# Kernel tuning notes

Measured on AMD Instinct MI355X. Metric: run time of the kernel, lower is better.

Reference implementation:

```python
import jax, jax.numpy as jnp
import numpy as np

B, C, N_OUT = 8, 64, 65536
N_IN = 262144  # unpooled (input) spatial size
K, P = 9, 4    # kernel_size, bilinear interp points


def setup_inputs() -> dict:
    key = jax.random.key(0)
    k1, k2, k3, k4 = jax.random.split(key, 4)
    x = jax.random.normal(k1, (B, C, N_OUT), dtype=jnp.float32)
    idx_mask = jax.random.randint(k2, (B, C, N_OUT), 0, K, dtype=jnp.int32)
    sample_map = jax.random.randint(k3, (N_OUT, K, P), 0, N_IN, dtype=jnp.int32)
    interp_weights = jax.random.uniform(k4, (N_OUT, K, P), dtype=jnp.float32)
    return {"x": x, "idx_mask": idx_mask, "sample_map": sample_map,
            "interp_weights": interp_weights}


def reference(x, idx_mask, sample_map, interp_weights):
    # x: [B,C,N_out] pooled values; idx_mask: [B,C,N_out] winning kernel tap
    # sample_map: [N_out,K,P] int indices into flattened unpooled domain
    # interp_weights: [N_out,K,P] interpolation weights
    b, c, n_out = x.shape
    o_idx = jnp.arange(n_out)[None, None, :]               # [1,1,N_out]
    sel_map = sample_map[o_idx, idx_mask]                  # [B,C,N_out,P]
    sel_w = interp_weights[o_idx, idx_mask]                # [B,C,N_out,P]
    contrib = sel_w * x[..., None]                         # [B,C,N_out,P]
    out = jnp.zeros((b, c, N_IN), dtype=x.dtype)
    bi = jnp.arange(b)[:, None, None, None]
    ci = jnp.arange(c)[None, :, None, None]
    out = out.at[bi, ci, sel_map].add(contrib)             # scatter-add unpool
    return out
```

## Files before the change

kernel.cpp:

```cpp
#include <hip/hip_runtime.h>

#define BB      8
#define CC      64
#define N_OUT   65536
#define N_IN    262144
#define KK      9
#define PP      4
#define NE      (N_OUT * KK * PP)
#define NPLANES 512
#define CHUNK   32
#define NCHUNKS (N_IN / CHUNK)
#define GTH     512
#define NW      (GTH / 64)
#define NFB     128
#define EPB     (NE / NFB)

#define WS_OFFSETS 0
#define WS_TOT     8208
#define WS_PRIV    16400
#define WS_HDR     (16400 + NFB * 8192)
#define WS_ENTR    (1064976 + N_OUT * KK)
#define WS_XK      (1654800 + 4 * NE)
#define WS_END     (11091984 + N_OUT * 512)

#define XKTILE 16
#define XPAD   520
__global__ __launch_bounds__(256) void k_xk(const float* __restrict__ x,
                                            const int*   __restrict__ idx,
                                            unsigned* __restrict__ xk,
                                            unsigned* __restrict__ hdr) {
    __shared__ float xs[XKTILE * XPAD];
    __shared__ unsigned char ks[XKTILE * XPAD];
    __shared__ unsigned ot[XKTILE * 512];
    __shared__ int cnt[XKTILE][12];
    __shared__ int cur[XKTILE][12];
    const int t = threadIdx.x;
    const int obase = blockIdx.x * XKTILE;

    for (int i = t; i < XKTILE * 12; i += 256) cnt[i / 12][i % 12] = 0;

    for (int i = t; i < 512 * (XKTILE / 4); i += 256) {
        int p = i >> 2, q = i & 3;
        const size_t g = (size_t)p * N_OUT + obase + 4 * q;
        float4 xv = *(const float4*)(x + g);
        int4   kv = *(const int4*)(idx + g);
        int b = (4 * q) * XPAD + p;
        xs[b] = xv.x; xs[b + XPAD] = xv.y; xs[b + 2 * XPAD] = xv.z; xs[b + 3 * XPAD] = xv.w;
        ks[b] = (unsigned char)kv.x; ks[b + XPAD] = (unsigned char)kv.y;
        ks[b + 2 * XPAD] = (unsigned char)kv.z; ks[b + 3 * XPAD] = (unsigned char)kv.w;
    }
    __syncthreads();
    for (int i = t; i < XKTILE * 512; i += 256) {
        int oo = i >> 9, p = i & 511;
        atomicAdd(&cnt[oo][ks[oo * XPAD + p]], 1);
    }
    __syncthreads();
    if (t < XKTILE) {
        int s = 0;
        for (int k = 0; k < KK; ++k) {
            int c = cnt[t][k];
            cur[t][k] = s;
            hdr[(size_t)(obase + t) * KK + k] = (unsigned)(s | (c << 16));
            s += c;
        }
    }
    __syncthreads();
    for (int i = t; i < XKTILE * 512; i += 256) {
        int oo = i >> 9, p = i & 511;
        int k = ks[oo * XPAD + p];
        int pos = atomicAdd(&cur[oo][k], 1);
        unsigned xb = __float_as_uint(xs[oo * XPAD + p]);
        ot[(oo << 9) + pos] = (xb & 0xFFFFFE00u) | (unsigned)p;
    }
    __syncthreads();
    for (int i = t; i < XKTILE * 128; i += 256) {
        int oo = i >> 7, c4 = i & 127;
        ((int4*)(xk + (((size_t)(obase + oo)) << 9)))[c4] = ((const int4*)(ot + (oo << 9)))[c4];
    }
}

__global__ __launch_bounds__(1024) void k_histA(const int* __restrict__ smap,
                                                int* __restrict__ priv) {
    __shared__ int h[8192];
    const int b = blockIdx.x;
    const int t = threadIdx.x;
    for (int i = t; i < 8192; i += 1024) h[i] = 0;
    __syncthreads();
    const int e0 = b * EPB;
    #pragma unroll 4
    for (int i = 0; i < EPB / 1024; ++i)
        atomicAdd(&h[smap[e0 + i * 1024 + t] >> 5], 1);
    __syncthreads();
    for (int i = t; i < 8192; i += 1024) priv[b * 8192 + i] = h[i];
}

__global__ __launch_bounds__(1024) void k_colscan(int* __restrict__ priv,
                                                  int* __restrict__ tot) {
    const int key = blockIdx.x * 1024 + threadIdx.x;
    int run = 0;
    for (int b = 0; b < NFB; ++b) {
        int* p = priv + b * 8192 + key;
        int v = *p; *p = run; run += v;
    }
    tot[key] = run;
}

__global__ __launch_bounds__(1024) void k_scan8k(const int* __restrict__ counts,
                                                 int* __restrict__ offsets) {
    __shared__ int sw[1024];
    const int t = threadIdx.x;
    int4 a = ((const int4*)counts)[2 * t];
    int4 b = ((const int4*)counts)[2 * t + 1];
    int s = a.x + a.y + a.z + a.w + b.x + b.y + b.z + b.w;
    sw[t] = s;
    __syncthreads();
    for (int off = 1; off < 1024; off <<= 1) {
        int v = (t >= off) ? sw[t - off] : 0;
        __syncthreads();
        sw[t] += v;
        __syncthreads();
    }
    int run = sw[t] - s;
    int vals[8] = {a.x, a.y, a.z, a.w, b.x, b.y, b.z, b.w};
    int o[8];
    #pragma unroll
    for (int q = 0; q < 8; ++q) { o[q] = run; run += vals[q]; }
    ((int4*)offsets)[2 * t]     = make_int4(o[0], o[1], o[2], o[3]);
    ((int4*)offsets)[2 * t + 1] = make_int4(o[4], o[5], o[6], o[7]);
    if (t == 1023) offsets[8192] = NE;
}

__global__ __launch_bounds__(1024) void k_fillB(const int* __restrict__ smap,
                                                const float* __restrict__ wts,
                                                const int* __restrict__ priv,
                                                const int* __restrict__ offsets,
                                                const unsigned* __restrict__ hdr,
                                                int4* __restrict__ entries) {
    __shared__ int cur[8192];
    const int b = blockIdx.x;
    const int t = threadIdx.x;
    for (int i = t; i < 8192; i += 1024) cur[i] = offsets[i] + priv[b * 8192 + i];
    __syncthreads();
    const int e0 = b * EPB;
    for (int i = 0; i < EPB / 1024; ++i) {
        const int e = e0 + i * 1024 + t;
        const int n = smap[e];
        const int o = e / 36;
        const int r = e - o * 36;
        const int k = r >> 2;
        const unsigned h = hdr[(size_t)o * KK + k];
        const int pos = atomicAdd(&cur[n >> 5], 1);
        entries[pos] = make_int4((o << 5) | (n & 31), __float_as_int(wts[e]), (int)h, 0);
    }
}

__global__ __launch_bounds__(GTH) void k_gather5(const int* __restrict__ offsets,
                                                 const int4* __restrict__ entries,
                                                 const unsigned* __restrict__ xk,
                                                 float* __restrict__ out) {
    __shared__ float acc[CHUNK * NPLANES];
    const int bid = blockIdx.x;
    const int c = (bid & 7) * (NCHUNKS / 8) + (bid >> 3);
    const int tid = threadIdx.x;
    const int lane = tid & 63;
    const int wid = tid >> 6;

    float4* a4 = (float4*)acc;
    for (int i = tid; i < CHUNK * NPLANES / 4; i += GTH) a4[i] = float4{0.f, 0.f, 0.f, 0.f};
    __syncthreads();

    const int j1 = offsets[c + 1];
    int j = offsets[c] + wid;
    int4 e = make_int4(0, 0, 0, 0);
    unsigned u0 = 0;
    bool have = (j < j1);
    if (have) {
        e = entries[j];
        int o = ((unsigned)e.x) >> 5;
        int st = e.z & 0xFFFF;
        int cn = ((unsigned)e.z) >> 16;
        if (lane < cn) u0 = xk[((size_t)o << 9) + st + lane];
    }
    while (have) {
        const int jn = j + NW;
        const bool hn = (jn < j1);
        int4 en = make_int4(0, 0, 0, 0);
        unsigned un = 0;
        if (hn) {
            en = entries[jn];
            int on = ((unsigned)en.x) >> 5;
            int stn = en.z & 0xFFFF;
            int cnn = ((unsigned)en.z) >> 16;
            if (lane < cnn) un = xk[((size_t)on << 9) + stn + lane];
        }
        {
            const int nl = e.x & 31;
            const float w = __int_as_float(e.y);
            const int cn = ((unsigned)e.z) >> 16;
            if (lane < cn) {
                int p = u0 & 511;
                float xv = __int_as_float(u0 & 0xFFFFFE00u);
                atomicAdd(&acc[(nl << 9) + (p ^ nl)], w * xv);
            }
            if (cn > 64) {
                const int o = ((unsigned)e.x) >> 5;
                const int st = e.z & 0xFFFF;
                for (int b = lane + 64; b < cn; b += 64) {
                    unsigned u = xk[((size_t)o << 9) + st + b];
                    int p = u & 511;
                    float xv = __int_as_float(u & 0xFFFFFE00u);
                    atomicAdd(&acc[(nl << 9) + (p ^ nl)], w * xv);
                }
            }
        }
        e = en; u0 = un; j = jn; have = hn;
    }
    __syncthreads();

    const int n0 = c << 5;
    for (int i = tid; i < CHUNK * NPLANES / 4; i += GTH) {
        const int p = i >> 3;
        const int nl = (i & 7) << 2;
        float4 v;
        v.x = acc[((nl + 0) << 9) + (p ^ (nl + 0))];
        v.y = acc[((nl + 1) << 9) + (p ^ (nl + 1))];
        v.z = acc[((nl + 2) << 9) + (p ^ (nl + 2))];
        v.w = acc[((nl + 3) << 9) + (p ^ (nl + 3))];
        *(float4*)(out + (size_t)p * N_IN + n0 + nl) = v;
    }
}

__global__ __launch_bounds__(256) void zero_kernel(float4* __restrict__ out, int n4) {
    int i = blockIdx.x * blockDim.x + threadIdx.x;
    int stride = gridDim.x * blockDim.x;
    const float4 z = {0.f, 0.f, 0.f, 0.f};
    for (; i < n4; i += stride) out[i] = z;
}

__global__ __launch_bounds__(256) void scatter_kernel(
    const float* __restrict__ x, const int* __restrict__ idx_mask,
    const int4* __restrict__ smap, const float4* __restrict__ wts,
    float* __restrict__ out)
{
    const int plane = blockIdx.x >> 8;
    const int o = ((blockIdx.x & 255) << 8) + threadIdx.x;
    const long ibase = (long)plane * N_OUT + o;
    const float xv = x[ibase];
    const int k = idx_mask[ibase];
    const int row = o * KK + k;
    const int4 m = smap[row];
    const float4 w = wts[row];
    float* op = out + (long)plane * N_IN;
    atomicAdd(op + m.x, w.x * xv);
    atomicAdd(op + m.y, w.y * xv);
    atomicAdd(op + m.z, w.z * xv);
    atomicAdd(op + m.w, w.w * xv);
}

extern "C" void kernel_launch(void* const* d_in, const int* in_sizes, int n_in,
                              void* d_out, int out_size, void* d_ws, size_t ws_size,
                              hipStream_t stream) {
    const float* x    = (const float*)d_in[0];
    const int*   idx  = (const int*)d_in[1];
    const int*   smap = (const int*)d_in[2];
    const float* wts  = (const float*)d_in[3];
    float* out = (float*)d_out;

    if (ws_size < (size_t)WS_END * 4) {
        zero_kernel<<<4096, 256, 0, stream>>>((float4*)out, out_size / 4);
        scatter_kernel<<<NPLANES * (N_OUT / 256), 256, 0, stream>>>(
            x, idx, (const int4*)smap, (const float4*)wts, out);
        return;
    }

    int* ws = (int*)d_ws;
    int* offsets   = ws + WS_OFFSETS;
    int* tot       = ws + WS_TOT;
    int* priv      = ws + WS_PRIV;
    unsigned* hdr  = (unsigned*)(ws + WS_HDR);
    int4* entries  = (int4*)(ws + WS_ENTR);
    unsigned* xk   = (unsigned*)(ws + WS_XK);

    k_xk<<<N_OUT / XKTILE, 256, 0, stream>>>(x, idx, xk, hdr);
    k_histA<<<NFB, 1024, 0, stream>>>(smap, priv);
    k_colscan<<<8, 1024, 0, stream>>>(priv, tot);
    k_scan8k<<<1, 1024, 0, stream>>>(tot, offsets);
    k_fillB<<<NFB, 1024, 0, stream>>>(smap, wts, priv, offsets, hdr, entries);
    k_gather5<<<NCHUNKS, GTH, 0, stream>>>(offsets, entries, xk, out);
}
```

Baseline: 1.012 ms.

## Halve gather chunk size, deepen entry prefetch, and retune LDS swizzle

Chunk width drops from 32 to 16 output columns, so the gather kernel's LDS accumulator halves (32KB) and more blocks can reside per CU, with launch bounds asking for 8. The histogram, scan and fill kernels are resized for twice as many keys. The gather loop now handles two entries per warp per iteration with a deeper software pipeline (entries two steps ahead, xk values one step ahead, including the second 64-lane slice), and the LDS swizzle is changed. The cost is more blocks, more per-chunk overhead, a larger scan, and higher register pressure.

```diff
diff --git a/kernel.cpp b/kernel.cpp
--- a/kernel.cpp
+++ b/kernel.cpp
@@ -8,20 +8,21 @@
 #define PP      4
 #define NE      (N_OUT * KK * PP)
 #define NPLANES 512
-#define CHUNK   32
+#define CHUNK   16
 #define NCHUNKS (N_IN / CHUNK)
+#define NKEY    NCHUNKS
 #define GTH     512
 #define NW      (GTH / 64)
 #define NFB     128
 #define EPB     (NE / NFB)
 
 #define WS_OFFSETS 0
-#define WS_TOT     8208
-#define WS_PRIV    16400
-#define WS_HDR     (16400 + NFB * 8192)
-#define WS_ENTR    (1064976 + N_OUT * KK)
-#define WS_XK      (1654800 + 4 * NE)
-#define WS_END     (11091984 + N_OUT * 512)
+#define WS_TOT     16400
+#define WS_PRIV    32784
+#define WS_HDR     (32784 + NFB * NKEY)
+#define WS_ENTR    (2129936 + N_OUT * KK)
+#define WS_XK      (2719760 + 4 * NE)
+#define WS_END     (12156944 + N_OUT * 512)
 
 #define XKTILE 16
 #define XPAD   520
@@ -81,17 +82,17 @@
 
 __global__ __launch_bounds__(1024) void k_histA(const int* __restrict__ smap,
                                                 int* __restrict__ priv) {
-    __shared__ int h[8192];
+    __shared__ int h[NKEY];
     const int b = blockIdx.x;
     const int t = threadIdx.x;
-    for (int i = t; i < 8192; i += 1024) h[i] = 0;
+    for (int i = t; i < NKEY; i += 1024) h[i] = 0;
     __syncthreads();
     const int e0 = b * EPB;
-    #pragma unroll 4
+    #pragma unroll 2
     for (int i = 0; i < EPB / 1024; ++i)
-        atomicAdd(&h[smap[e0 + i * 1024 + t] >> 5], 1);
-    __syncthreads();
-    for (int i = t; i < 8192; i += 1024) priv[b * 8192 + i] = h[i];
+        atomicAdd(&h[smap[e0 + i * 1024 + t] >> 4], 1);
+    __syncthreads();
+    for (int i = t; i < NKEY; i += 1024) priv[b * NKEY + i] = h[i];
 }
 
 __global__ __launch_bounds__(1024) void k_colscan(int* __restrict__ priv,
@@ -99,19 +100,25 @@
     const int key = blockIdx.x * 1024 + threadIdx.x;
     int run = 0;
     for (int b = 0; b < NFB; ++b) {
-        int* p = priv + b * 8192 + key;
+        int* p = priv + b * NKEY + key;
         int v = *p; *p = run; run += v;
     }
     tot[key] = run;
 }
 
-__global__ __launch_bounds__(1024) void k_scan8k(const int* __restrict__ counts,
-                                                 int* __restrict__ offsets) {
+__global__ __launch_bounds__(1024) void k_scan16k(const int* __restrict__ tot,
+                                                  int* __restrict__ offsets) {
     __shared__ int sw[1024];
     const int t = threadIdx.x;
-    int4 a = ((const int4*)counts)[2 * t];
-    int4 b = ((const int4*)counts)[2 * t + 1];
-    int s = a.x + a.y + a.z + a.w + b.x + b.y + b.z + b.w;
+    int4 q0 = ((const int4*)tot)[4 * t + 0];
+    int4 q1 = ((const int4*)tot)[4 * t + 1];
+    int4 q2 = ((const int4*)tot)[4 * t + 2];
+    int4 q3 = ((const int4*)tot)[4 * t + 3];
+    int vals[16] = {q0.x, q0.y, q0.z, q0.w, q1.x, q1.y, q1.z, q1.w,
+                    q2.x, q2.y, q2.z, q2.w, q3.x, q3.y, q3.z, q3.w};
+    int s = 0;
+    #pragma unroll
+    for (int i = 0; i < 16; ++i) s += vals[i];
     sw[t] = s;
     __syncthreads();
     for (int off = 1; off < 1024; off <<= 1) {
@@ -121,13 +128,14 @@
         __syncthreads();
     }
     int run = sw[t] - s;
-    int vals[8] = {a.x, a.y, a.z, a.w, b.x, b.y, b.z, b.w};
-    int o[8];
+    int o[16];
     #pragma unroll
-    for (int q = 0; q < 8; ++q) { o[q] = run; run += vals[q]; }
-    ((int4*)offsets)[2 * t]     = make_int4(o[0], o[1], o[2], o[3]);
-    ((int4*)offsets)[2 * t + 1] = make_int4(o[4], o[5], o[6], o[7]);
-    if (t == 1023) offsets[8192] = NE;
+    for (int i = 0; i < 16; ++i) { o[i] = run; run += vals[i]; }
+    ((int4*)offsets)[4 * t + 0] = make_int4(o[0], o[1], o[2], o[3]);
+    ((int4*)offsets)[4 * t + 1] = make_int4(o[4], o[5], o[6], o[7]);
+    ((int4*)offsets)[4 * t + 2] = make_int4(o[8], o[9], o[10], o[11]);
+    ((int4*)offsets)[4 * t + 3] = make_int4(o[12], o[13], o[14], o[15]);
+    if (t == 1023) offsets[NKEY] = NE;
 }
 
 __global__ __launch_bounds__(1024) void k_fillB(const int* __restrict__ smap,
@@ -136,10 +144,10 @@
                                                 const int* __restrict__ offsets,
                                                 const unsigned* __restrict__ hdr,
                                                 int4* __restrict__ entries) {
-    __shared__ int cur[8192];
+    __shared__ int cur[NKEY];
     const int b = blockIdx.x;
     const int t = threadIdx.x;
-    for (int i = t; i < 8192; i += 1024) cur[i] = offsets[i] + priv[b * 8192 + i];
+    for (int i = t; i < NKEY; i += 1024) cur[i] = offsets[i] + priv[b * NKEY + i];
     __syncthreads();
     const int e0 = b * EPB;
     for (int i = 0; i < EPB / 1024; ++i) {
@@ -149,15 +157,16 @@
         const int r = e - o * 36;
         const int k = r >> 2;
         const unsigned h = hdr[(size_t)o * KK + k];
-        const int pos = atomicAdd(&cur[n >> 5], 1);
-        entries[pos] = make_int4((o << 5) | (n & 31), __float_as_int(wts[e]), (int)h, 0);
-    }
-}
-
-__global__ __launch_bounds__(GTH) void k_gather5(const int* __restrict__ offsets,
-                                                 const int4* __restrict__ entries,
-                                                 const unsigned* __restrict__ xk,
-                                                 float* __restrict__ out) {
+        const int pos = atomicAdd(&cur[n >> 4], 1);
+        entries[pos] = make_int4((o << 4) | (n & 15), __float_as_int(wts[e]), (int)h, 0);
+    }
+}
+
+#define SWZ(p, nl) ((p) ^ ((nl) << 1))
+__global__ __launch_bounds__(GTH, 8) void k_gather6(const int* __restrict__ offsets,
+                                                    const int4* __restrict__ entries,
+                                                    const unsigned* __restrict__ xk,
+                                                    float* __restrict__ out) {
     __shared__ float acc[CHUNK * NPLANES];
     const int bid = blockIdx.x;
     const int c = (bid & 7) * (NCHUNKS / 8) + (bid >> 3);
@@ -170,62 +179,104 @@
     __syncthreads();
 
     const int j1 = offsets[c + 1];
-    int j = offsets[c] + wid;
-    int4 e = make_int4(0, 0, 0, 0);
-    unsigned u0 = 0;
-    bool have = (j < j1);
-    if (have) {
-        e = entries[j];
-        int o = ((unsigned)e.x) >> 5;
-        int st = e.z & 0xFFFF;
-        int cn = ((unsigned)e.z) >> 16;
-        if (lane < cn) u0 = xk[((size_t)o << 9) + st + lane];
-    }
-    while (have) {
-        const int jn = j + NW;
-        const bool hn = (jn < j1);
-        int4 en = make_int4(0, 0, 0, 0);
-        unsigned un = 0;
-        if (hn) {
-            en = entries[jn];
-            int on = ((unsigned)en.x) >> 5;
-            int stn = en.z & 0xFFFF;
-            int cnn = ((unsigned)en.z) >> 16;
-            if (lane < cnn) un = xk[((size_t)on << 9) + stn + lane];
-        }
-        {
-            const int nl = e.x & 31;
-            const float w = __int_as_float(e.y);
-            const int cn = ((unsigned)e.z) >> 16;
+    int jA = offsets[c] + wid;
+
+    int4 eA0 = {0,0,0,0}, eA1 = {0,0,0,0};
+    if (jA < j1)      eA0 = entries[jA];
+    if (jA + NW < j1) eA1 = entries[jA + NW];
+    unsigned xA0 = 0, xA1 = 0, xA0b = 0, xA1b = 0;
+    if (jA < j1) {
+        int o = ((unsigned)eA0.x) >> 4, st = eA0.z & 0xFFFF, cn = ((unsigned)eA0.z) >> 16;
+        const unsigned* r = xk + ((size_t)o << 9) + st;
+        if (lane < cn) xA0 = r[lane];
+        if (cn > 64 && lane + 64 < cn) xA0b = r[lane + 64];
+    }
+    if (jA + NW < j1) {
+        int o = ((unsigned)eA1.x) >> 4, st = eA1.z & 0xFFFF, cn = ((unsigned)eA1.z) >> 16;
+        const unsigned* r = xk + ((size_t)o << 9) + st;
+        if (lane < cn) xA1 = r[lane];
+        if (cn > 64 && lane + 64 < cn) xA1b = r[lane + 64];
+    }
+    int jB = jA + 2 * NW;
+    int4 eB0 = {0,0,0,0}, eB1 = {0,0,0,0};
+    if (jB < j1)      eB0 = entries[jB];
+    if (jB + NW < j1) eB1 = entries[jB + NW];
+
+    while (jA < j1) {
+        unsigned xB0 = 0, xB1 = 0, xB0b = 0, xB1b = 0;
+        if (jB < j1) {
+            int o = ((unsigned)eB0.x) >> 4, st = eB0.z & 0xFFFF, cn = ((unsigned)eB0.z) >> 16;
+            const unsigned* r = xk + ((size_t)o << 9) + st;
+            if (lane < cn) xB0 = r[lane];
+            if (cn > 64 && lane + 64 < cn) xB0b = r[lane + 64];
+        }
+        if (jB + NW < j1) {
+            int o = ((unsigned)eB1.x) >> 4, st = eB1.z & 0xFFFF, cn = ((unsigned)eB1.z) >> 16;
+            const unsigned* r = xk + ((size_t)o << 9) + st;
+            if (lane < cn) xB1 = r[lane];
+            if (cn > 64 && lane + 64 < cn) xB1b = r[lane + 64];
+        }
+        const int jC = jB + 2 * NW;
+        int4 eC0 = {0,0,0,0}, eC1 = {0,0,0,0};
+        if (jC < j1)      eC0 = entries[jC];
+        if (jC + NW < j1) eC1 = entries[jC + NW];
+
+        if (jA < j1) {
+            const int nl = eA0.x & 15, cn = ((unsigned)eA0.z) >> 16;
+            const float w = __int_as_float(eA0.y);
             if (lane < cn) {
-                int p = u0 & 511;
-                float xv = __int_as_float(u0 & 0xFFFFFE00u);
-                atomicAdd(&acc[(nl << 9) + (p ^ nl)], w * xv);
-            }
-            if (cn > 64) {
-                const int o = ((unsigned)e.x) >> 5;
-                const int st = e.z & 0xFFFF;
-                for (int b = lane + 64; b < cn; b += 64) {
+                int p = xA0 & 511;
+                atomicAdd(&acc[(nl << 9) + SWZ(p, nl)], w * __int_as_float(xA0 & 0xFFFFFE00u));
+            }
+            if (cn > 64 && lane + 64 < cn) {
+                int p = xA0b & 511;
+                atomicAdd(&acc[(nl << 9) + SWZ(p, nl)], w * __int_as_float(xA0b & 0xFFFFFE00u));
+            }
+            if (cn > 128) {
+                const int o = ((unsigned)eA0.x) >> 4, st = eA0.z & 0xFFFF;
+                for (int b = lane + 128; b < cn; b += 64) {
                     unsigned u = xk[((size_t)o << 9) + st + b];
                     int p = u & 511;
-                    float xv = __int_as_float(u & 0xFFFFFE00u);
-                    atomicAdd(&acc[(nl << 9) + (p ^ nl)], w * xv);
+                    atomicAdd(&acc[(nl << 9) + SWZ(p, nl)], w * __int_as_float(u & 0xFFFFFE00u));
                 }
             }
         }
-        e = en; u0 = un; j = jn; have = hn;
-    }
-    __syncthreads();
-
-    const int n0 = c << 5;
+        if (jA + NW < j1) {
+            const int nl = eA1.x & 15, cn = ((unsigned)eA1.z) >> 16;
+            const float w = __int_as_float(eA1.y);
+            if (lane < cn) {
+                int p = xA1 & 511;
+                atomicAdd(&acc[(nl << 9) + SWZ(p, nl)], w * __int_as_float(xA1 & 0xFFFFFE00u));
+            }
+            if (cn > 64 && lane + 64 < cn) {
+                int p = xA1b & 511;
+                atomicAdd(&acc[(nl << 9) + SWZ(p, nl)], w * __int_as_float(xA1b & 0xFFFFFE00u));
+            }
+            if (cn > 128) {
+                const int o = ((unsigned)eA1.x) >> 4, st = eA1.z & 0xFFFF;
+                for (int b = lane + 128; b < cn; b += 64) {
+                    unsigned u = xk[((size_t)o << 9) + st + b];
+                    int p = u & 511;
+                    atomicAdd(&acc[(nl << 9) + SWZ(p, nl)], w * __int_as_float(u & 0xFFFFFE00u));
+                }
+            }
+        }
+        eA0 = eB0; eA1 = eB1;
+        xA0 = xB0; xA1 = xB1; xA0b = xB0b; xA1b = xB1b;
+        jA = jB;
+        eB0 = eC0; eB1 = eC1; jB = jC;
+    }
+    __syncthreads();
+
+    const int n0 = c << 4;
     for (int i = tid; i < CHUNK * NPLANES / 4; i += GTH) {
-        const int p = i >> 3;
-        const int nl = (i & 7) << 2;
+        const int p = i >> 2;
+        const int nl = (i & 3) << 2;
         float4 v;
-        v.x = acc[((nl + 0) << 9) + (p ^ (nl + 0))];
-        v.y = acc[((nl + 1) << 9) + (p ^ (nl + 1))];
-        v.z = acc[((nl + 2) << 9) + (p ^ (nl + 2))];
-        v.w = acc[((nl + 3) << 9) + (p ^ (nl + 3))];
+        v.x = acc[((nl + 0) << 9) + SWZ(p, nl + 0)];
+        v.y = acc[((nl + 1) << 9) + SWZ(p, nl + 1)];
+        v.z = acc[((nl + 2) << 9) + SWZ(p, nl + 2)];
+        v.w = acc[((nl + 3) << 9) + SWZ(p, nl + 3)];
         *(float4*)(out + (size_t)p * N_IN + n0 + nl) = v;
     }
 }
@@ -283,8 +334,8 @@
 
     k_xk<<<N_OUT / XKTILE, 256, 0, stream>>>(x, idx, xk, hdr);
     k_histA<<<NFB, 1024, 0, stream>>>(smap, priv);
-    k_colscan<<<8, 1024, 0, stream>>>(priv, tot);
-    k_scan8k<<<1, 1024, 0, stream>>>(tot, offsets);
+    k_colscan<<<16, 1024, 0, stream>>>(priv, tot);
+    k_scan16k<<<1, 1024, 0, stream>>>(tot, offsets);
     k_fillB<<<NFB, 1024, 0, stream>>>(smap, wts, priv, offsets, hdr, entries);
-    k_gather5<<<NCHUNKS, GTH, 0, stream>>>(offsets, entries, xk, out);
-}
+    k_gather6<<<NCHUNKS, GTH, 0, stream>>>(offsets, entries, xk, out);
+}
```

Result: faster. 965.6 us (-4.6%).
